# Kernel tuning notes

Measured on AMD Instinct MI355X. Metric: run time of the kernel, lower is better.

## Reference

```python
import jax, jax.numpy as jnp
import numpy as np

B, S, D = 4, 2048, 1024
H, DK, DV = 16, 64, 64


def setup_inputs() -> dict:
    key = jax.random.key(0)
    ks = jax.random.split(key, 7)
    scale = 0.02
    emb = jax.random.normal(ks[0], (B, S, D), dtype=jnp.float32)
    # per-head projection weights stacked over heads: [H, D, DK/DV]
    Wq = jax.random.normal(ks[1], (H, D, DK), dtype=jnp.float32) * scale
    Wk = jax.random.normal(ks[2], (H, D, DK), dtype=jnp.float32) * scale
    Wv = jax.random.normal(ks[3], (H, D, DV), dtype=jnp.float32) * scale
    # output projection (nn.Linear(d_model, d_model)): weight [D, D] (input-major) + bias
    Wo = jax.random.normal(ks[4], (D, D), dtype=jnp.float32) * scale
    bo = jax.random.normal(ks[5], (D,), dtype=jnp.float32) * scale
    return {"emb": emb, "Wq": Wq, "Wk": Wk, "Wv": Wv, "Wo": Wo, "bo": bo}


def reference(emb, Wq, Wk, Wv, Wo, bo):
    # Per-head projections, batched over heads: [B,H,S,dk]
    q = jnp.einsum("bsd,hdk->bhsk", emb, Wq)
    k = jnp.einsum("bsd,hdk->bhsk", emb, Wk)
    v = jnp.einsum("bsd,hdv->bhsv", emb, Wv)
    # Scaled dot-product with causal mask (bool_mask=True)
    scores = jnp.einsum("bhqk,bhsk->bhqs", q, k) * (DK ** -0.5)  # [B,H,S,S]
    causal = jnp.tril(jnp.ones((S, S), dtype=bool))
    scores = jnp.where(causal, scores, jnp.finfo(scores.dtype).min)
    attn = jax.nn.softmax(scores, axis=-1)
    out = jnp.einsum("bhqs,bhsv->bhqv", attn, v)  # [B,H,S,DV]
    # concat heads -> [B,S,H*DV] == [B,S,D]
    out = out.transpose(0, 2, 1, 3).reshape(B, S, H * DV)
    # output projection; dropout=0.0 -> identity
    return out @ Wo + bo
```

## Files before the change

### kernel.cpp

```cpp
#include <hip/hip_runtime.h>
#include <hip/hip_bf16.h>


typedef __attribute__((ext_vector_type(8))) short bf16x8;
typedef __attribute__((ext_vector_type(4))) float f32x4;
typedef __attribute__((ext_vector_type(4))) unsigned int u32x4;
typedef __attribute__((ext_vector_type(2))) unsigned int u32x2;

#define MFMA16(a, b, c) __builtin_amdgcn_mfma_f32_16x16x32_bf16((a), (b), (c), 0, 0, 0)

#define LOG2E 1.44269504088896340736f
#define BIG_NEG (-3.0e38f)
#define DEFER_THR 10.0f

__device__ __forceinline__ unsigned short f2bf(float f) {
  union { float f; unsigned int i; } x; x.f = f;
  unsigned int lsb = (x.i >> 16) & 1;
  x.i += 0x7fffu + lsb;
  return (unsigned short)(x.i >> 16);
}

__device__ __forceinline__ unsigned int cvtpk(float lo, float hi) {
  unsigned int r;
  asm("v_cvt_pk_bf16_f32 %0, %1, %2" : "=v"(r) : "v"(lo), "v"(hi));
  return r;
}

__device__ __forceinline__ void gl16(const unsigned short* g, void* l) {
  __builtin_amdgcn_global_load_lds(
      (const __attribute__((address_space(1))) unsigned int*)g,
      (__attribute__((address_space(3))) unsigned int*)l, 16, 0, 0);
}

__global__ void wtrans_kernel(const float* __restrict__ in,
                              unsigned short* __restrict__ out, int R, int C) {
  __shared__ unsigned short tile[32][33];
  const int bz = blockIdx.z;
  const int c0 = blockIdx.x * 32, r0 = blockIdx.y * 32;
  const float* ip = in + (size_t)bz * R * C;
  unsigned short* op = out + (size_t)bz * R * C;
  const int tx = threadIdx.x, ty = threadIdx.y;
#pragma unroll
  for (int i = 0; i < 32; i += 8)
    tile[ty + i][tx] = f2bf(ip[(size_t)(r0 + ty + i) * C + (c0 + tx)]);
  __syncthreads();
#pragma unroll
  for (int i = 0; i < 32; i += 8)
    op[(size_t)(c0 + ty + i) * R + (r0 + tx)] = tile[tx][ty + i];
}

__global__ __launch_bounds__(256)
void embconv_kernel(const float* __restrict__ in, unsigned short* __restrict__ out) {
  const int i = blockIdx.x * 256 + threadIdx.x;
  const float4 a = ((const float4*)in)[2 * i];
  const float4 b = ((const float4*)in)[2 * i + 1];
  union { unsigned short u[8]; u32x4 v; } p;
  p.u[0] = f2bf(a.x); p.u[1] = f2bf(a.y); p.u[2] = f2bf(a.z); p.u[3] = f2bf(a.w);
  p.u[4] = f2bf(b.x); p.u[5] = f2bf(b.y); p.u[6] = f2bf(b.z); p.u[7] = f2bf(b.w);
  ((u32x4*)out)[i] = p.v;
}

__global__ __launch_bounds__(256)
void qkv_kernel(const unsigned short* __restrict__ embB,
                const unsigned short* __restrict__ WqT,
                const unsigned short* __restrict__ WkT,
                const unsigned short* __restrict__ WvT,
                unsigned short* __restrict__ QG,
                unsigned short* __restrict__ KG,
                unsigned short* __restrict__ VtG) {
  const int nwg = gridDim.x;
  const int wg = blockIdx.x;
  const int swz = (wg & 7) * (nwg >> 3) + (wg >> 3);
  const int mb = swz / 24;
  const int rem = swz - mb * 24;
  const int t = rem >> 3;
  const int m0 = mb * 128;
  const int n0 = (rem & 7) * 128;
  const int b = m0 >> 11;
  const int sloc = m0 & 2047;
  const unsigned short* Wt =
      (t == 0 ? WqT : (t == 1 ? WkT : WvT)) + (size_t)(n0 >> 6) * 64 * 1024;

  __shared__ __align__(16) unsigned short As[128 * 32];
  __shared__ __align__(16) unsigned short Bs[128 * 32];

  const int tid = threadIdx.x;
  const int lane = tid & 63, w = tid >> 6;
  const int q4 = lane >> 4, l16 = lane & 15;
  const int lr = lane >> 2, lc = (lane & 3) * 8;

  f32x4 acc[4][4] = {};

  const unsigned short* ga0 = &embB[(size_t)(m0 + w * 32 + lr) * 1024 + lc];
  const unsigned short* ga1 = ga0 + 16 * 1024;
  const unsigned short* gb0 = &Wt[(size_t)(w * 32 + lr) * 1024 + lc];
  const unsigned short* gb1 = gb0 + 16 * 1024;
  char* la0 = (char*)As + w * 2048;
  char* lb0 = (char*)Bs + w * 2048;

  for (int k0 = 0; k0 < 1024; k0 += 32) {
    __syncthreads();
    gl16(ga0 + k0, la0);
    gl16(ga1 + k0, la0 + 1024);
    gl16(gb0 + k0, lb0);
    gl16(gb1 + k0, lb0 + 1024);
    __syncthreads();

    const unsigned short* PA = (t == 2) ? Bs : As;
    const unsigned short* PB = (t == 2) ? As : Bs;

    bf16x8 af[4], bfr[4];
#pragma unroll
    for (int ms = 0; ms < 4; ++ms)
      af[ms] = *(const bf16x8*)&PA[((w >> 1) * 64 + ms * 16 + l16) * 32 + q4 * 8];
#pragma unroll
    for (int js = 0; js < 4; ++js)
      bfr[js] = *(const bf16x8*)&PB[((w & 1) * 64 + js * 16 + l16) * 32 + q4 * 8];
    __builtin_amdgcn_s_setprio(1);
#pragma unroll
    for (int ms = 0; ms < 4; ++ms)
#pragma unroll
      for (int js = 0; js < 4; ++js)
        acc[ms][js] = MFMA16(af[ms], bfr[js], acc[ms][js]);
    __builtin_amdgcn_s_setprio(0);
  }

  if (t < 2) {
    unsigned short* outp = (t == 0) ? QG : KG;
    const float osc = (t == 0) ? (0.125f * LOG2E) : 1.0f;
    const int h = (n0 >> 6) + (w & 1);
    const size_t hb = (size_t)(b * 16 + h) * 2048;
#pragma unroll
    for (int ms = 0; ms < 4; ++ms)
#pragma unroll
      for (int js = 0; js < 4; ++js) {
        const int c = js * 16 + l16;
#pragma unroll
        for (int r = 0; r < 4; ++r) {
          const int s = sloc + (w >> 1) * 64 + ms * 16 + q4 * 4 + r;
          outp[(hb + s) * 64 + c] = f2bf(acc[ms][js][r] * osc);
        }
      }
  } else {
    const int h = (n0 >> 6) + (w >> 1);
    const size_t hb = (size_t)(b * 16 + h) * 64;
#pragma unroll
    for (int ms = 0; ms < 4; ++ms)
#pragma unroll
      for (int js = 0; js < 4; ++js) {
        const int s = sloc + (w & 1) * 64 + js * 16 + l16;
#pragma unroll
        for (int r = 0; r < 4; ++r) {
          const int c = ms * 16 + q4 * 4 + r;
          VtG[(hb + c) * 2048 + s] = f2bf(acc[ms][js][r]);
        }
      }
  }
}

__global__ __launch_bounds__(512)
void flash_kernel(const unsigned short* __restrict__ QG,
                  const unsigned short* __restrict__ KG,
                  const unsigned short* __restrict__ VtG,
                  unsigned short* __restrict__ ObG) {
  const int bh = blockIdx.x;
  const int y = blockIdx.y;
  const int k4 = y >> 2, y0 = y & 3;
  const int t = k4 + 4 * ((y0 + k4) & 3);
  const int q0 = t * 128;
  const int tid = threadIdx.x;
  const int lane = tid & 63, w = tid >> 6;
  const int wp = w & 3;
  const int q4 = lane >> 4, l16 = lane & 15;
  const int qw = q0 + w * 16;
  const int jlim = q0 + ((w >= 4) ? 64 : 0);
  const int jlimB = q0 + 64;

  const unsigned short* Qp = QG + ((size_t)bh * 2048 + qw) * 64;
  const unsigned short* Kp = KG + (size_t)bh * 2048 * 64;
  const unsigned short* Vp = VtG + (size_t)bh * 64 * 2048;

  const bf16x8 qf0 = *(const bf16x8*)&Qp[(size_t)l16 * 64 + q4 * 8];
  const bf16x8 qf1 = *(const bf16x8*)&Qp[(size_t)l16 * 64 + 32 + q4 * 8];

  __shared__ __align__(16) unsigned short Ks[64 * 64];
  __shared__ __align__(16) unsigned short Vs[64 * 64];
  __shared__ __align__(16) unsigned short Plds[8 * 16 * 64];

  f32x4 oacc[4] = {};
  float m_i = BIG_NEG, l_part = 0.f;

  const int sr = tid >> 3, sc = (tid & 7) * 8;
  const int sdst = sr * 64 + (((tid & 7) ^ (sr & 7)) * 8);
  u32x4 kreg = *(const u32x4*)&Kp[(size_t)sr * 64 + sc];
  u32x4 vreg = *(const u32x4*)&Vp[(size_t)sr * 2048 + sc];

  const int x7 = l16 & 7;
  const int ks0 = (q4 ^ x7) * 8;
  const int ks1 = ((4 + q4) ^ x7) * 8;
  const int prow = (w * 16 + l16) * 64;

  for (int j0 = 0; j0 <= jlimB; j0 += 64) {
    *(u32x4*)&Ks[sdst] = kreg;
    *(u32x4*)&Vs[sdst] = vreg;
    __syncthreads();

    if (j0 + 64 <= jlimB) {
      const int jn = j0 + 64;
      kreg = *(const u32x4*)&Kp[(size_t)(jn + sr) * 64 + sc];
      vreg = *(const u32x4*)&Vp[(size_t)sr * 2048 + jn + sc];
    }

    if (j0 <= jlim) {
      f32x4 sacc[4] = {};
      __builtin_amdgcn_s_setprio(1);
#pragma unroll
      for (int js = 0; js < 4; ++js) {
        const int krow = (js * 16 + l16) * 64;
        const bf16x8 kf0 = *(const bf16x8*)&Ks[krow + ks0];
        const bf16x8 kf1 = *(const bf16x8*)&Ks[krow + ks1];
        sacc[js] = MFMA16(kf0, qf0, sacc[js]);
        sacc[js] = MFMA16(kf1, qf1, sacc[js]);
      }
      __builtin_amdgcn_s_setprio(0);

      float mloc = BIG_NEG;
      if (j0 == jlim) {
        const int qrel = wp * 16 + l16;
#pragma unroll
        for (int js = 0; js < 4; ++js)
#pragma unroll
          for (int r = 0; r < 4; ++r) {
            const int krel = js * 16 + q4 * 4 + r;
            float v = sacc[js][r];
            if (krel > qrel) v = BIG_NEG;
            sacc[js][r] = v;
            mloc = fmaxf(mloc, v);
          }
      } else {
#pragma unroll
        for (int js = 0; js < 4; ++js)
#pragma unroll
          for (int r = 0; r < 4; ++r) mloc = fmaxf(mloc, sacc[js][r]);
      }
      mloc = fmaxf(mloc, __shfl_xor(mloc, 16, 64));
      mloc = fmaxf(mloc, __shfl_xor(mloc, 32, 64));

      if (__any(mloc > m_i + DEFER_THR)) {
        const float mnew = fmaxf(m_i, mloc);
        const float alpha = __builtin_amdgcn_exp2f(m_i - mnew);
        m_i = mnew;
        l_part *= alpha;
#pragma unroll
        for (int js = 0; js < 4; ++js)
#pragma unroll
          for (int r = 0; r < 4; ++r) oacc[js][r] *= alpha;
      }

#pragma unroll
      for (int js = 0; js < 4; ++js)
#pragma unroll
        for (int r = 0; r < 4; ++r) {
          const float p = __builtin_amdgcn_exp2f(sacc[js][r] - m_i);
          sacc[js][r] = p;
          l_part += p;
        }

#pragma unroll
      for (int js = 0; js < 4; ++js) {
        u32x2 pk;
        pk[0] = cvtpk(sacc[js][0], sacc[js][1]);
        pk[1] = cvtpk(sacc[js][2], sacc[js][3]);
        const int pslot = (((js * 2 + (q4 >> 1)) ^ x7) * 8) + ((q4 & 1) * 4);
        *(u32x2*)&Plds[prow + pslot] = pk;
      }

      asm volatile("" ::: "memory");

      const int prd = (w * 16 + l16) * 64;
      const bf16x8 pf0 = *(const bf16x8*)&Plds[prd + ks0];
      const bf16x8 pf1 = *(const bf16x8*)&Plds[prd + ks1];

      __builtin_amdgcn_s_setprio(1);
#pragma unroll
      for (int js = 0; js < 4; ++js) {
        const int vrow = (js * 16 + l16) * 64;
        const bf16x8 vf0 = *(const bf16x8*)&Vs[vrow + ks0];
        const bf16x8 vf1 = *(const bf16x8*)&Vs[vrow + ks1];
        oacc[js] = MFMA16(vf0, pf0, oacc[js]);
        oacc[js] = MFMA16(vf1, pf1, oacc[js]);
      }
      __builtin_amdgcn_s_setprio(0);
    }
    __syncthreads();
  }

  float l_i = l_part;
  l_i += __shfl_xor(l_i, 16, 64);
  l_i += __shfl_xor(l_i, 32, 64);

  const int b = bh >> 4, h = bh & 15;
  const int q = qw + l16;
  const float rl = 1.0f / l_i;
  unsigned short* orow = ObG + ((size_t)b * 2048 + q) * 1024 + h * 64;
#pragma unroll
  for (int js = 0; js < 4; ++js) {
    u32x2 ok;
    ok[0] = cvtpk(oacc[js][0] * rl, oacc[js][1] * rl);
    ok[1] = cvtpk(oacc[js][2] * rl, oacc[js][3] * rl);
    *(u32x2*)&orow[js * 16 + q4 * 4] = ok;
  }
}

__global__ __launch_bounds__(256)
void oproj_kernel(const unsigned short* __restrict__ ObG,
                  const unsigned short* __restrict__ WoT,
                  const float* __restrict__ bo,
                  float* __restrict__ outG) {
  const int nwg = gridDim.x;
  const int wg = blockIdx.x;
  const int swz = (wg & 7) * (nwg >> 3) + (wg >> 3);
  const int m0 = (swz >> 3) * 128;
  const int n0 = (swz & 7) * 128;

  __shared__ __align__(16) unsigned short As[128 * 32];
  __shared__ __align__(16) unsigned short Bs[128 * 32];

  const int tid = threadIdx.x;
  const int lane = tid & 63, w = tid >> 6;
  const int q4 = lane >> 4, l16 = lane & 15;
  const int lr = lane >> 2, lc = (lane & 3) * 8;

  f32x4 acc[4][4] = {};

  const unsigned short* ga0 = &ObG[(size_t)(m0 + w * 32 + lr) * 1024 + lc];
  const unsigned short* ga1 = ga0 + 16 * 1024;
  const unsigned short* gb0 = &WoT[(size_t)(n0 + w * 32 + lr) * 1024 + lc];
  const unsigned short* gb1 = gb0 + 16 * 1024;
  char* la0 = (char*)As + w * 2048;
  char* lb0 = (char*)Bs + w * 2048;

  for (int k0 = 0; k0 < 1024; k0 += 32) {
    __syncthreads();
    gl16(ga0 + k0, la0);
    gl16(ga1 + k0, la0 + 1024);
    gl16(gb0 + k0, lb0);
    gl16(gb1 + k0, lb0 + 1024);
    __syncthreads();

    bf16x8 af[4], bfr[4];
#pragma unroll
    for (int ms = 0; ms < 4; ++ms)
      af[ms] = *(const bf16x8*)&As[((w >> 1) * 64 + ms * 16 + l16) * 32 + q4 * 8];
#pragma unroll
    for (int js = 0; js < 4; ++js)
      bfr[js] = *(const bf16x8*)&Bs[((w & 1) * 64 + js * 16 + l16) * 32 + q4 * 8];
    __builtin_amdgcn_s_setprio(1);
#pragma unroll
    for (int ms = 0; ms < 4; ++ms)
#pragma unroll
      for (int js = 0; js < 4; ++js)
        acc[ms][js] = MFMA16(af[ms], bfr[js], acc[ms][js]);
    __builtin_amdgcn_s_setprio(0);
  }

#pragma unroll
  for (int js = 0; js < 4; ++js) {
    const int col = n0 + (w & 1) * 64 + js * 16 + l16;
    const float bias = bo[col];
#pragma unroll
    for (int ms = 0; ms < 4; ++ms)
#pragma unroll
      for (int r = 0; r < 4; ++r) {
        const int row = m0 + (w >> 1) * 64 + ms * 16 + q4 * 4 + r;
        outG[(size_t)row * 1024 + col] = acc[ms][js][r] + bias;
      }
  }
}

extern "C" void kernel_launch(void* const* d_in, const int* in_sizes, int n_in,
                              void* d_out, int out_size, void* d_ws, size_t ws_size,
                              hipStream_t stream) {
  const float* emb = (const float*)d_in[0];
  const float* Wq  = (const float*)d_in[1];
  const float* Wk  = (const float*)d_in[2];
  const float* Wv  = (const float*)d_in[3];
  const float* Wo  = (const float*)d_in[4];
  const float* bo  = (const float*)d_in[5];
  float* out = (float*)d_out;

  char* ws = (char*)d_ws;
  const size_t MB = 1024 * 1024;

  const int nb = (ws_size >= 72 * MB) ? 4 : (ws_size >= 40 * MB) ? 2 : 1;

  unsigned short* WqT = (unsigned short*)(ws + 0 * MB);
  unsigned short* WkT = (unsigned short*)(ws + 2 * MB);
  unsigned short* WvT = (unsigned short*)(ws + 4 * MB);
  unsigned short* WoT = (unsigned short*)(ws + 6 * MB);
  unsigned short* QG  = (unsigned short*)(ws + 8 * MB);
  unsigned short* KG  = (unsigned short*)(ws + (8 + 4 * nb) * MB);
  unsigned short* VtG = (unsigned short*)(ws + (8 + 8 * nb) * MB);
  unsigned short* ObG = (unsigned short*)(ws + (8 + 12 * nb) * MB);

  const dim3 tb(32, 8, 1);
  wtrans_kernel<<<dim3(2, 32, 16), tb, 0, stream>>>(Wq, WqT, 1024, 64);
  wtrans_kernel<<<dim3(2, 32, 16), tb, 0, stream>>>(Wk, WkT, 1024, 64);
  wtrans_kernel<<<dim3(2, 32, 16), tb, 0, stream>>>(Wv, WvT, 1024, 64);
  wtrans_kernel<<<dim3(32, 32, 1), tb, 0, stream>>>(Wo, WoT, 1024, 1024);

  for (int g = 0; g < 4; g += nb) {
    const float* embG = emb + (size_t)g * 2048 * 1024;
    float* outG = out + (size_t)g * 2048 * 1024;
    unsigned short* embB = ObG;
    embconv_kernel<<<dim3(nb * 1024), 256, 0, stream>>>(embG, embB);
    qkv_kernel<<<dim3(24 * 16 * nb), 256, 0, stream>>>(embB, WqT, WkT, WvT, QG, KG, VtG);
    flash_kernel<<<dim3(16 * nb, 16), 512, 0, stream>>>(QG, KG, VtG, ObG);
    oproj_kernel<<<dim3(8 * 16 * nb), 256, 0, stream>>>(ObG, WoT, bo, outG);
  }
}
```

Measured before the change: 265.5 us.

## Double K-tile depth in QKV and output GEMMs with XOR-swizzled LDS, merge weight transposes

The QKV and output-projection GEMMs now stage 64-wide K slices per iteration instead of 32, using an XOR-swizzled LDS layout. This halves the number of barrier pairs per tile and is meant to avoid LDS bank conflicts on the fragment reads. The three per-head weight transpose launches are merged into one kernel to cut launch overhead. The flash kernel's P read offset is switched to reuse the already-computed prow index. Doubling LDS use per block could lower occupancy.

```diff
diff --git a/kernel.cpp b/kernel.cpp
--- a/kernel.cpp
+++ b/kernel.cpp
@@ -32,21 +32,40 @@
       (__attribute__((address_space(3))) unsigned int*)l, 16, 0, 0);
 }
 
+__global__ void wtrans3_kernel(const float* __restrict__ Wq,
+                               const float* __restrict__ Wk,
+                               const float* __restrict__ Wv,
+                               unsigned short* __restrict__ Oq,
+                               unsigned short* __restrict__ Ok,
+                               unsigned short* __restrict__ Ov) {
+  __shared__ unsigned short tile[32][33];
+  const int bz = blockIdx.z;
+  const int which = bz >> 4, h = bz & 15;
+  const float* ip = (which == 0 ? Wq : which == 1 ? Wk : Wv) + (size_t)h * 1024 * 64;
+  unsigned short* op = (which == 0 ? Oq : which == 1 ? Ok : Ov) + (size_t)h * 1024 * 64;
+  const int c0 = blockIdx.x * 32, r0 = blockIdx.y * 32;
+  const int tx = threadIdx.x, ty = threadIdx.y;
+#pragma unroll
+  for (int i = 0; i < 32; i += 8)
+    tile[ty + i][tx] = f2bf(ip[(size_t)(r0 + ty + i) * 64 + (c0 + tx)]);
+  __syncthreads();
+#pragma unroll
+  for (int i = 0; i < 32; i += 8)
+    op[(size_t)(c0 + ty + i) * 1024 + (r0 + tx)] = tile[tx][ty + i];
+}
+
 __global__ void wtrans_kernel(const float* __restrict__ in,
                               unsigned short* __restrict__ out, int R, int C) {
   __shared__ unsigned short tile[32][33];
-  const int bz = blockIdx.z;
   const int c0 = blockIdx.x * 32, r0 = blockIdx.y * 32;
-  const float* ip = in + (size_t)bz * R * C;
-  unsigned short* op = out + (size_t)bz * R * C;
   const int tx = threadIdx.x, ty = threadIdx.y;
 #pragma unroll
   for (int i = 0; i < 32; i += 8)
-    tile[ty + i][tx] = f2bf(ip[(size_t)(r0 + ty + i) * C + (c0 + tx)]);
+    tile[ty + i][tx] = f2bf(in[(size_t)(r0 + ty + i) * C + (c0 + tx)]);
   __syncthreads();
 #pragma unroll
   for (int i = 0; i < 32; i += 8)
-    op[(size_t)(c0 + ty + i) * R + (r0 + tx)] = tile[tx][ty + i];
+    out[(size_t)(c0 + ty + i) * R + (r0 + tx)] = tile[tx][ty + i];
 }
 
 __global__ __launch_bounds__(256)
@@ -81,48 +100,53 @@
   const unsigned short* Wt =
       (t == 0 ? WqT : (t == 1 ? WkT : WvT)) + (size_t)(n0 >> 6) * 64 * 1024;
 
-  __shared__ __align__(16) unsigned short As[128 * 32];
-  __shared__ __align__(16) unsigned short Bs[128 * 32];
+  __shared__ __align__(16) unsigned short As[128 * 64];
+  __shared__ __align__(16) unsigned short Bs[128 * 64];
 
   const int tid = threadIdx.x;
   const int lane = tid & 63, w = tid >> 6;
   const int q4 = lane >> 4, l16 = lane & 15;
-  const int lr = lane >> 2, lc = (lane & 3) * 8;
+  const int x7 = l16 & 7;
 
   f32x4 acc[4][4] = {};
 
-  const unsigned short* ga0 = &embB[(size_t)(m0 + w * 32 + lr) * 1024 + lc];
-  const unsigned short* ga1 = ga0 + 16 * 1024;
-  const unsigned short* gb0 = &Wt[(size_t)(w * 32 + lr) * 1024 + lc];
-  const unsigned short* gb1 = gb0 + 16 * 1024;
-  char* la0 = (char*)As + w * 2048;
-  char* lb0 = (char*)Bs + w * 2048;
-
-  for (int k0 = 0; k0 < 1024; k0 += 32) {
-    __syncthreads();
-    gl16(ga0 + k0, la0);
-    gl16(ga1 + k0, la0 + 1024);
-    gl16(gb0 + k0, lb0);
-    gl16(gb1 + k0, lb0 + 1024);
+  const int grow = w * 32 + (lane >> 3);
+  const int gcol = (((lane & 7) ^ ((lane >> 3) & 7)) * 8);
+  const unsigned short* gaB = &embB[(size_t)(m0 + grow) * 1024 + gcol];
+  const unsigned short* gbB = &Wt[(size_t)grow * 1024 + gcol];
+  char* laB = (char*)As + (w * 32) * 128;
+  char* lbB = (char*)Bs + (w * 32) * 128;
+
+  for (int k0 = 0; k0 < 1024; k0 += 64) {
+    __syncthreads();
+#pragma unroll
+    for (int i = 0; i < 4; ++i) {
+      gl16(gaB + (size_t)i * 8 * 1024 + k0, laB + i * 1024);
+      gl16(gbB + (size_t)i * 8 * 1024 + k0, lbB + i * 1024);
+    }
     __syncthreads();
 
     const unsigned short* PA = (t == 2) ? Bs : As;
     const unsigned short* PB = (t == 2) ? As : Bs;
 
-    bf16x8 af[4], bfr[4];
-#pragma unroll
-    for (int ms = 0; ms < 4; ++ms)
-      af[ms] = *(const bf16x8*)&PA[((w >> 1) * 64 + ms * 16 + l16) * 32 + q4 * 8];
-#pragma unroll
-    for (int js = 0; js < 4; ++js)
-      bfr[js] = *(const bf16x8*)&PB[((w & 1) * 64 + js * 16 + l16) * 32 + q4 * 8];
-    __builtin_amdgcn_s_setprio(1);
-#pragma unroll
-    for (int ms = 0; ms < 4; ++ms)
+#pragma unroll
+    for (int kk = 0; kk < 2; ++kk) {
+      const int slot = ((kk * 4 + q4) ^ x7) * 8;
+      bf16x8 af[4], bfr[4];
+#pragma unroll
+      for (int ms = 0; ms < 4; ++ms)
+        af[ms] = *(const bf16x8*)&PA[((w >> 1) * 64 + ms * 16 + l16) * 64 + slot];
 #pragma unroll
       for (int js = 0; js < 4; ++js)
-        acc[ms][js] = MFMA16(af[ms], bfr[js], acc[ms][js]);
-    __builtin_amdgcn_s_setprio(0);
+        bfr[js] = *(const bf16x8*)&PB[((w & 1) * 64 + js * 16 + l16) * 64 + slot];
+      __builtin_amdgcn_s_setprio(1);
+#pragma unroll
+      for (int ms = 0; ms < 4; ++ms)
+#pragma unroll
+        for (int js = 0; js < 4; ++js)
+          acc[ms][js] = MFMA16(af[ms], bfr[js], acc[ms][js]);
+      __builtin_amdgcn_s_setprio(0);
+    }
   }
 
   if (t < 2) {
@@ -277,9 +301,8 @@
 
       asm volatile("" ::: "memory");
 
-      const int prd = (w * 16 + l16) * 64;
-      const bf16x8 pf0 = *(const bf16x8*)&Plds[prd + ks0];
-      const bf16x8 pf1 = *(const bf16x8*)&Plds[prd + ks1];
+      const bf16x8 pf0 = *(const bf16x8*)&Plds[prow + ks0];
+      const bf16x8 pf1 = *(const bf16x8*)&Plds[prow + ks1];
 
       __builtin_amdgcn_s_setprio(1);
 #pragma unroll
@@ -323,45 +346,50 @@
   const int m0 = (swz >> 3) * 128;
   const int n0 = (swz & 7) * 128;
 
-  __shared__ __align__(16) unsigned short As[128 * 32];
-  __shared__ __align__(16) unsigned short Bs[128 * 32];
+  __shared__ __align__(16) unsigned short As[128 * 64];
+  __shared__ __align__(16) unsigned short Bs[128 * 64];
 
   const int tid = threadIdx.x;
   const int lane = tid & 63, w = tid >> 6;
   const int q4 = lane >> 4, l16 = lane & 15;
-  const int lr = lane >> 2, lc = (lane & 3) * 8;
+  const int x7 = l16 & 7;
 
   f32x4 acc[4][4] = {};
 
-  const unsigned short* ga0 = &ObG[(size_t)(m0 + w * 32 + lr) * 1024 + lc];
-  const unsigned short* ga1 = ga0 + 16 * 1024;
-  const unsigned short* gb0 = &WoT[(size_t)(n0 + w * 32 + lr) * 1024 + lc];
-  const unsigned short* gb1 = gb0 + 16 * 1024;
-  char* la0 = (char*)As + w * 2048;
-  char* lb0 = (char*)Bs + w * 2048;
-
-  for (int k0 = 0; k0 < 1024; k0 += 32) {
-    __syncthreads();
-    gl16(ga0 + k0, la0);
-    gl16(ga1 + k0, la0 + 1024);
-    gl16(gb0 + k0, lb0);
-    gl16(gb1 + k0, lb0 + 1024);
-    __syncthreads();
-
-    bf16x8 af[4], bfr[4];
-#pragma unroll
-    for (int ms = 0; ms < 4; ++ms)
-      af[ms] = *(const bf16x8*)&As[((w >> 1) * 64 + ms * 16 + l16) * 32 + q4 * 8];
-#pragma unroll
-    for (int js = 0; js < 4; ++js)
-      bfr[js] = *(const bf16x8*)&Bs[((w & 1) * 64 + js * 16 + l16) * 32 + q4 * 8];
-    __builtin_amdgcn_s_setprio(1);
-#pragma unroll
-    for (int ms = 0; ms < 4; ++ms)
+  const int grow = w * 32 + (lane >> 3);
+  const int gcol = (((lane & 7) ^ ((lane >> 3) & 7)) * 8);
+  const unsigned short* gaB = &ObG[(size_t)(m0 + grow) * 1024 + gcol];
+  const unsigned short* gbB = &WoT[(size_t)(n0 + grow) * 1024 + gcol];
+  char* laB = (char*)As + (w * 32) * 128;
+  char* lbB = (char*)Bs + (w * 32) * 128;
+
+  for (int k0 = 0; k0 < 1024; k0 += 64) {
+    __syncthreads();
+#pragma unroll
+    for (int i = 0; i < 4; ++i) {
+      gl16(gaB + (size_t)i * 8 * 1024 + k0, laB + i * 1024);
+      gl16(gbB + (size_t)i * 8 * 1024 + k0, lbB + i * 1024);
+    }
+    __syncthreads();
+
+#pragma unroll
+    for (int kk = 0; kk < 2; ++kk) {
+      const int slot = ((kk * 4 + q4) ^ x7) * 8;
+      bf16x8 af[4], bfr[4];
+#pragma unroll
+      for (int ms = 0; ms < 4; ++ms)
+        af[ms] = *(const bf16x8*)&As[((w >> 1) * 64 + ms * 16 + l16) * 64 + slot];
 #pragma unroll
       for (int js = 0; js < 4; ++js)
-        acc[ms][js] = MFMA16(af[ms], bfr[js], acc[ms][js]);
-    __builtin_amdgcn_s_setprio(0);
+        bfr[js] = *(const bf16x8*)&Bs[((w & 1) * 64 + js * 16 + l16) * 64 + slot];
+      __builtin_amdgcn_s_setprio(1);
+#pragma unroll
+      for (int ms = 0; ms < 4; ++ms)
+#pragma unroll
+        for (int js = 0; js < 4; ++js)
+          acc[ms][js] = MFMA16(af[ms], bfr[js], acc[ms][js]);
+      __builtin_amdgcn_s_setprio(0);
+    }
   }
 
 #pragma unroll
@@ -404,9 +432,7 @@
   unsigned short* ObG = (unsigned short*)(ws + (8 + 12 * nb) * MB);
 
   const dim3 tb(32, 8, 1);
-  wtrans_kernel<<<dim3(2, 32, 16), tb, 0, stream>>>(Wq, WqT, 1024, 64);
-  wtrans_kernel<<<dim3(2, 32, 16), tb, 0, stream>>>(Wk, WkT, 1024, 64);
-  wtrans_kernel<<<dim3(2, 32, 16), tb, 0, stream>>>(Wv, WvT, 1024, 64);
+  wtrans3_kernel<<<dim3(2, 32, 48), tb, 0, stream>>>(Wq, Wk, Wv, WqT, WkT, WvT);
   wtrans_kernel<<<dim3(32, 32, 1), tb, 0, stream>>>(Wo, WoT, 1024, 1024);
 
   for (int g = 0; g < 4; g += nb) {
```

Result: faster. 250.6 us (-5.6%).
